# Kernel tuning notes

Hardware: AMD Instinct MI355X
Metric: run time of the kernel (lower is better)

Reference implementation:

```python
import jax, jax.numpy as jnp
import numpy as np

B, N, E = 4, 8192, 65536
OBS, H, OUT, NOUT = 128, 256, 1024, 18


def setup_inputs() -> dict:
    key = jax.random.key(0)
    ks = jax.random.split(key, 8)
    nodes = jax.random.normal(ks[0], (B, N, OBS), dtype=jnp.float32)
    edges = jax.random.randint(ks[1], (B, 2, E), 0, N, dtype=jnp.int64)
    # Glorot-ish init for weights
    W0 = jax.random.normal(ks[2], (OBS, H), dtype=jnp.float32) / np.float32(np.sqrt(OBS))
    W1 = jax.random.normal(ks[3], (H, OUT), dtype=jnp.float32) / np.float32(np.sqrt(H))
    W_logit = jax.random.normal(ks[4], (OUT, NOUT), dtype=jnp.float32) / np.float32(np.sqrt(OUT))
    W_val = jax.random.normal(ks[5], (OUT, 1), dtype=jnp.float32) / np.float32(np.sqrt(OUT))
    return {
        "nodes": nodes, "edges": edges,
        "W0": W0, "b0": jnp.zeros((H,), jnp.float32),
        "W1": W1, "b1": jnp.zeros((OUT,), jnp.float32),
        "W_logit": W_logit, "b_logit": jnp.zeros((NOUT,), jnp.float32),
        "W_val": W_val, "b_val": jnp.zeros((1,), jnp.float32),
    }


def _gcn_layer(x, src, dst, W, b, n):
    # PyG GCNConv: out = D^{-1/2} (A + I) D^{-1/2} X W + b   (self-loops already in src/dst)
    h = x @ W                                                     # [N, F_out]
    deg = jax.ops.segment_sum(jnp.ones(src.shape, jnp.float32), dst, num_segments=n)
    dinv = jnp.where(deg > 0, jax.lax.rsqrt(deg), 0.0)            # deg^{-1/2}
    norm = dinv[src] * dinv[dst]                                  # [Etot]
    msg = h[src] * norm[:, None]                                  # gather + normalize
    agg = jax.ops.segment_sum(msg, dst, num_segments=n)           # scatter-add
    return agg + b


def reference(nodes, edges, W0, b0, W1, b1, W_logit, b_logit, W_val, b_val):
    n = nodes.shape[1]
    loops = jnp.arange(n, dtype=edges.dtype)  # self-loops, added by GCNConv

    def per_graph(x, ei):
        src = jnp.concatenate([ei[0], loops])
        dst = jnp.concatenate([ei[1], loops])
        h = jax.nn.relu(_gcn_layer(x, src, dst, W0, b0, n))
        # (original applies F.dropout here; omitted for a deterministic reference)
        h = jax.nn.relu(_gcn_layer(h, src, dst, W1, b1, n))
        return h

    out = jax.vmap(per_graph)(nodes, edges)        # [B, N, OUT]
    logits = out @ W_logit + b_logit               # [B, N, NOUT]
    values = (out @ W_val + b_val)[..., 0]         # [B, N]
    return logits, values
```

## Files before the change

kernel.cpp:

```cpp
#include <hip/hip_runtime.h>
#include <hip/hip_bf16.h>

#define BB   4
#define NN   8192
#define EE   65536
#define FOBS 128
#define FH   256
#define FOUT 1024
#define NLOG 18
#define BKT  64

typedef __attribute__((ext_vector_type(8))) short frag8;
typedef __attribute__((ext_vector_type(4))) float f32x4;

__device__ __forceinline__ ushort f2b(float v) {
    __hip_bfloat16 h = __float2bfloat16(v);
    return *reinterpret_cast<ushort*>(&h);
}
__device__ __forceinline__ float blo(uint u) { return __uint_as_float(u << 16); }
__device__ __forceinline__ float bhi(uint u) { return __uint_as_float(u & 0xffff0000u); }

__device__ __forceinline__ void gld16(const void* g, void* l) {
    __builtin_amdgcn_global_load_lds(
        (const __attribute__((address_space(1))) unsigned*)g,
        (__attribute__((address_space(3))) unsigned*)l, 16, 0, 0);
}

#define XB2_N  (BB * NN * FOBS / 2)
#define W0_N   (FOBS * FH)
#define W1_N   (FH * FOUT)
#define WH_N   (19 * FOUT)
#define CUR_N  (BB * NN)
#define OUTI_N (BB * NN * 19)
#define PREP_TOTAL (XB2_N + W0_N + W1_N + WH_N + CUR_N + OUTI_N)

__global__ void prep_kernel(const float* __restrict__ nodes, uint* __restrict__ xb,
                            const float* __restrict__ W0, ushort* __restrict__ W0T,
                            const float* __restrict__ W1, ushort* __restrict__ W1T,
                            const float* __restrict__ Wl, const float* __restrict__ Wv,
                            ushort* __restrict__ WT19, int* __restrict__ cursor,
                            const float* __restrict__ bl, const float* __restrict__ bv,
                            float* __restrict__ out_logits, float* __restrict__ out_values) {
    int idx = blockIdx.x * blockDim.x + threadIdx.x;
    if (idx < XB2_N) {
        float2 xx = ((const float2*)nodes)[idx];
        xb[idx] = (uint)f2b(xx.x) | ((uint)f2b(xx.y) << 16);
        return;
    }
    idx -= XB2_N;
    if (idx < W0_N) {
        int n = idx / FOBS, k = idx - n * FOBS;
        W0T[idx] = f2b(W0[(size_t)k * FH + n]);
        return;
    }
    idx -= W0_N;
    if (idx < W1_N) {
        int n = idx / FH, k = idx - n * FH;
        W1T[idx] = f2b(W1[(size_t)k * FOUT + n]);
        return;
    }
    idx -= W1_N;
    if (idx < WH_N) {
        int o = idx >> 10, k = idx & (FOUT - 1);
        WT19[idx] = f2b((o < NLOG) ? Wl[(size_t)k * NLOG + o] : Wv[k]);
        return;
    }
    idx -= WH_N;
    if (idx < CUR_N) { cursor[idx] = 0; return; }
    idx -= CUR_N;
    if (idx < OUTI_N) {
        int gn = idx / 19, o = idx - gn * 19;
        if (o < NLOG) out_logits[(size_t)gn * NLOG + o] = bl[o];
        else          out_values[gn] = bv[0];
    }
}

__global__ void bucket_fill(const int* __restrict__ edges, int* __restrict__ cursor,
                            ushort* __restrict__ bucket) {
    int blk = blockIdx.x;
    int xcd = blk & 7;
    int g = xcd >> 1;
    int chunk = (blk >> 3) * 2 + (xcd & 1);
    int e = chunk * 256 + threadIdx.x;
    const int* src = edges + (size_t)g * 2 * EE;
    const int* dst = src + EE;
    int d = dst[e];
    int slot = atomicAdd(&cursor[(size_t)g * NN + d], 1);
    if (slot < BKT) bucket[((size_t)g * NN + d) * BKT + slot] = (ushort)src[e];
}

__global__ __launch_bounds__(256) void gather_agg_b128(
    const uint4* __restrict__ xb4_all, const int* __restrict__ cnt_all,
    const ushort* __restrict__ bucket, uint4* __restrict__ agg_all)
{
    int blk = blockIdx.x;
    int xcd = blk & 7;
    int g = xcd >> 1;
    int chunk = (blk >> 3) * 2 + (xcd & 1);
    int wv = threadIdx.x >> 6, lane = threadIdx.x & 63;
    int n = chunk * 4 + wv;
    int q = lane >> 4, sub = lane & 15;
    const uint4* xb4 = xb4_all + (size_t)g * NN * 16;
    const int* cnt = cnt_all + (size_t)g * NN;
    const ushort* bkt = bucket + ((size_t)g * NN + n) * BKT;

    int cn = cnt[n];
    float wn = rsqrtf((float)cn + 1.0f);
    int total = min(cn, BKT) + 1;

    float acc[8] = {};
    for (int base = 0; base < total; base += 8) {
#pragma unroll
        for (int j = 0; j < 2; ++j) {
            int vr = base + q + 4 * j;
            bool ok = vr < total;
            int src = (!ok || vr == 0) ? n : (int)bkt[vr - 1];
            float w = ok ? rsqrtf((float)cnt[src] + 1.0f) * wn : 0.0f;
            uint4 r = xb4[(size_t)src * 16 + sub];
            acc[0] += w * blo(r.x); acc[1] += w * bhi(r.x);
            acc[2] += w * blo(r.y); acc[3] += w * bhi(r.y);
            acc[4] += w * blo(r.z); acc[5] += w * bhi(r.z);
            acc[6] += w * blo(r.w); acc[7] += w * bhi(r.w);
        }
    }
#pragma unroll
    for (int e = 0; e < 8; ++e) {
        acc[e] += __shfl_xor(acc[e], 16);
        acc[e] += __shfl_xor(acc[e], 32);
    }
    if (lane < 16) {
        uint4 o;
        o.x = (uint)f2b(acc[0]) | ((uint)f2b(acc[1]) << 16);
        o.y = (uint)f2b(acc[2]) | ((uint)f2b(acc[3]) << 16);
        o.z = (uint)f2b(acc[4]) | ((uint)f2b(acc[5]) << 16);
        o.w = (uint)f2b(acc[6]) | ((uint)f2b(acc[7]) << 16);
        agg_all[((size_t)g * NN + n) * 16 + sub] = o;
    }
}

__global__ __launch_bounds__(256) void gather_agg_b256(
    const uint4* __restrict__ xb4_all, const int* __restrict__ cnt_all,
    const ushort* __restrict__ bucket, uint4* __restrict__ agg_all)
{
    int blk = blockIdx.x;
    int xcd = blk & 7;
    int g = xcd >> 1;
    int chunk = (blk >> 3) * 2 + (xcd & 1);
    int wv = threadIdx.x >> 6, lane = threadIdx.x & 63;
    int n = chunk * 4 + wv;
    int h = lane >> 5, sub = lane & 31;
    const uint4* xb4 = xb4_all + (size_t)g * NN * 32;
    const int* cnt = cnt_all + (size_t)g * NN;
    const ushort* bkt = bucket + ((size_t)g * NN + n) * BKT;

    int cn = cnt[n];
    float wn = rsqrtf((float)cn + 1.0f);
    int total = min(cn, BKT) + 1;

    float acc[8] = {};
    for (int base = 0; base < total; base += 8) {
#pragma unroll
        for (int j = 0; j < 4; ++j) {
            int vr = base + h + 2 * j;
            bool ok = vr < total;
            int src = (!ok || vr == 0) ? n : (int)bkt[vr - 1];
            float w = ok ? rsqrtf((float)cnt[src] + 1.0f) * wn : 0.0f;
            uint4 r = xb4[(size_t)src * 32 + sub];
            acc[0] += w * blo(r.x); acc[1] += w * bhi(r.x);
            acc[2] += w * blo(r.y); acc[3] += w * bhi(r.y);
            acc[4] += w * blo(r.z); acc[5] += w * bhi(r.z);
            acc[6] += w * blo(r.w); acc[7] += w * bhi(r.w);
        }
    }
#pragma unroll
    for (int e = 0; e < 8; ++e)
        acc[e] += __shfl_xor(acc[e], 32);
    if (lane < 32) {
        uint4 o;
        o.x = (uint)f2b(acc[0]) | ((uint)f2b(acc[1]) << 16);
        o.y = (uint)f2b(acc[2]) | ((uint)f2b(acc[3]) << 16);
        o.z = (uint)f2b(acc[4]) | ((uint)f2b(acc[5]) << 16);
        o.w = (uint)f2b(acc[6]) | ((uint)f2b(acc[7]) << 16);
        agg_all[((size_t)g * NN + n) * 32 + sub] = o;
    }
}

__global__ __launch_bounds__(256) void mfma_gemm(
    const ushort* __restrict__ A_all, const ushort* __restrict__ BT,
    const float* __restrict__ bias, ushort* __restrict__ C_all,
    int M, int N, int K, int relu)
{
    __shared__ __align__(16) ushort As[128 * 64];
    __shared__ __align__(16) ushort Bs[128 * 64];

    int g = blockIdx.z;
    const ushort* A = A_all + (size_t)g * M * K;
    ushort* C = C_all + (size_t)g * M * N;

    int t = threadIdx.x;
    int bn = blockIdx.x, bm = blockIdx.y;
    int lane = t & 63, w = t >> 6;
    int wm = w >> 1, wn = w & 1;
    int l15 = lane & 15, quad = lane >> 4;

    f32x4 acc[4][4] = {};

    const char* Abase = (const char*)(A + (size_t)(bm * 128) * K);
    const char* Bbase = (const char*)(BT + (size_t)(bn * 128) * K);
    size_t rstride = (size_t)K * 2;

    int rsub = lane >> 3;
    int colb = (lane & 7) * 16;

    for (int k0 = 0; k0 < K; k0 += 64) {
#pragma unroll
        for (int c = 0; c < 4; ++c) {
            int grp = c * 4 + w;
            int row = grp * 8 + rsub;
            int gcol = k0 * 2 + (colb ^ ((row & 7) << 4));
            gld16(Abase + (size_t)row * rstride + gcol, (char*)As + grp * 1024);
            gld16(Bbase + (size_t)row * rstride + gcol, (char*)Bs + grp * 1024);
        }
        __syncthreads();
#pragma unroll
        for (int kk = 0; kk < 64; kk += 32) {
            frag8 af[4], bf[4];
#pragma unroll
            for (int i = 0; i < 4; ++i) {
                int r = wm * 64 + i * 16 + l15;
                int cb = (kk * 2 + quad * 16) ^ ((r & 7) << 4);
                af[i] = *(const frag8*)((const char*)As + r * 128 + cb);
            }
#pragma unroll
            for (int j = 0; j < 4; ++j) {
                int r = wn * 64 + j * 16 + l15;
                int cb = (kk * 2 + quad * 16) ^ ((r & 7) << 4);
                bf[j] = *(const frag8*)((const char*)Bs + r * 128 + cb);
            }
#pragma unroll
            for (int i = 0; i < 4; ++i)
#pragma unroll
                for (int j = 0; j < 4; ++j)
                    acc[i][j] = __builtin_amdgcn_mfma_f32_16x16x32_bf16(af[i], bf[j], acc[i][j], 0, 0, 0);
        }
        __syncthreads();
    }

#pragma unroll
    for (int i = 0; i < 4; ++i) {
#pragma unroll
        for (int j = 0; j < 4; ++j) {
            int col = bn * 128 + wn * 64 + j * 16 + l15;
            float bcol = bias[col];
#pragma unroll
            for (int r = 0; r < 4; ++r) {
                int row = bm * 128 + wm * 64 + i * 16 + quad * 4 + r;
                float v = acc[i][j][r] + bcol;
                if (relu) v = fmaxf(v, 0.0f);
                C[(size_t)row * N + col] = f2b(v);
            }
        }
    }
}

__global__ __launch_bounds__(256) void gemm2_heads(
    const ushort* __restrict__ hagg_all,
    const ushort* __restrict__ W1T,
    const float*  __restrict__ b1,
    const ushort* __restrict__ WT19,
    float* __restrict__ out_logits,
    float* __restrict__ out_values)
{
    __shared__ __align__(16) ushort smem[128 * 136];
    __shared__ __align__(16) ushort wt[20][136];

    char* AsB = (char*)smem;
    char* BsB = (char*)smem + 16384;
    ushort* Ct = smem;

    int bm = blockIdx.x, sp = blockIdx.y, g = blockIdx.z;
    int t = threadIdx.x;
    int lane = t & 63, w = t >> 6;
    int wm = w >> 1, wn = w & 1;
    int l15 = lane & 15, quad = lane >> 4;

    const char* A0 = (const char*)(hagg_all + ((size_t)g * NN + bm * 128) * FH);

    if (t < 136) wt[19][t] = 0;

    int rsub = lane >> 3;
    int colb = (lane & 7) * 16;

    f32x4 hacc[2][2] = {};

    for (int bi = 0; bi < 4; ++bi) {
        int bn = sp * 4 + bi;
        __syncthreads();

        for (int idx = t; idx < 19 * 16; idx += 256) {
            int row = idx >> 4, c8 = (idx & 15) * 8;
            *(uint4*)&wt[row][c8] = *(const uint4*)(WT19 + (size_t)row * FOUT + bn * 128 + c8);
        }

        f32x4 acc[4][4] = {};
        const char* Bbase = (const char*)(W1T + (size_t)(bn * 128) * FH);

        for (int k0 = 0; k0 < FH; k0 += 64) {
#pragma unroll
            for (int c = 0; c < 4; ++c) {
                int grp = c * 4 + w;
                int row = grp * 8 + rsub;
                int gcol = k0 * 2 + (colb ^ ((row & 7) << 4));
                gld16(A0 + (size_t)row * (FH * 2) + gcol, AsB + grp * 1024);
                gld16(Bbase + (size_t)row * (FH * 2) + gcol, BsB + grp * 1024);
            }
            __syncthreads();
#pragma unroll
            for (int kk = 0; kk < 64; kk += 32) {
                frag8 af[4], bf[4];
#pragma unroll
                for (int i = 0; i < 4; ++i) {
                    int r = wm * 64 + i * 16 + l15;
                    int cb = (kk * 2 + quad * 16) ^ ((r & 7) << 4);
                    af[i] = *(const frag8*)(AsB + r * 128 + cb);
                }
#pragma unroll
                for (int j = 0; j < 4; ++j) {
                    int r = wn * 64 + j * 16 + l15;
                    int cb = (kk * 2 + quad * 16) ^ ((r & 7) << 4);
                    bf[j] = *(const frag8*)(BsB + r * 128 + cb);
                }
#pragma unroll
                for (int i = 0; i < 4; ++i)
#pragma unroll
                    for (int j = 0; j < 4; ++j)
                        acc[i][j] = __builtin_amdgcn_mfma_f32_16x16x32_bf16(af[i], bf[j], acc[i][j], 0, 0, 0);
            }
            __syncthreads();
        }

#pragma unroll
        for (int j = 0; j < 4; ++j) {
            int colL = wn * 64 + j * 16 + l15;
            float bcol = b1[bn * 128 + colL];
#pragma unroll
            for (int i = 0; i < 4; ++i) {
                int rowL = wm * 64 + i * 16 + quad * 4;
#pragma unroll
                for (int r = 0; r < 4; ++r) {
                    float v = fmaxf(acc[i][j][r] + bcol, 0.0f);
                    Ct[(size_t)(rowL + r) * 136 + colL] = f2b(v);
                }
            }
        }
        __syncthreads();

        int r1 = (l15 < 3) ? (16 + l15) : 19;
#pragma unroll
        for (int kk = 0; kk < 128; kk += 32) {
            frag8 b0 = *(const frag8*)&wt[l15][kk + quad * 8];
            frag8 bO = *(const frag8*)&wt[r1][kk + quad * 8];
#pragma unroll
            for (int mt = 0; mt < 2; ++mt) {
                int row = (w * 2 + mt) * 16 + l15;
                frag8 af = *(const frag8*)&Ct[(size_t)row * 136 + kk + quad * 8];
                hacc[mt][0] = __builtin_amdgcn_mfma_f32_16x16x32_bf16(af, b0, hacc[mt][0], 0, 0, 0);
                hacc[mt][1] = __builtin_amdgcn_mfma_f32_16x16x32_bf16(af, bO, hacc[mt][1], 0, 0, 0);
            }
        }
    }

#pragma unroll
    for (int mt = 0; mt < 2; ++mt) {
#pragma unroll
        for (int r = 0; r < 4; ++r) {
            int node = bm * 128 + (w * 2 + mt) * 16 + quad * 4 + r;
            size_t gn = (size_t)g * NN + node;
            atomicAdd(&out_logits[gn * NLOG + l15], hacc[mt][0][r]);
            if (l15 < 2)       atomicAdd(&out_logits[gn * NLOG + 16 + l15], hacc[mt][1][r]);
            else if (l15 == 2) atomicAdd(&out_values[gn], hacc[mt][1][r]);
        }
    }
}

extern "C" void kernel_launch(void* const* d_in, const int* in_sizes, int n_in,
                              void* d_out, int out_size, void* d_ws, size_t ws_size,
                              hipStream_t stream) {
    const float* nodes = (const float*)d_in[0];
    const int*   edges = (const int*)d_in[1];
    const float* W0 = (const float*)d_in[2];
    const float* b0 = (const float*)d_in[3];
    const float* W1 = (const float*)d_in[4];
    const float* b1 = (const float*)d_in[5];
    const float* Wl = (const float*)d_in[6];
    const float* bl = (const float*)d_in[7];
    const float* Wv = (const float*)d_in[8];
    const float* bv = (const float*)d_in[9];

    float* out_logits = (float*)d_out;
    float* out_values = out_logits + (size_t)BB * NN * NLOG;

    char* ws = (char*)d_ws;
    int*    cursor  = (int*)(ws);
    ushort* W0T     = (ushort*)(ws + (128 << 10));
    ushort* W1T     = (ushort*)(ws + (192 << 10));
    ushort* WT19    = (ushort*)(ws + (704 << 10));
    uint*   xb      = (uint*)(ws + (1u << 20));
    ushort* bucket  = (ushort*)(ws + (9u << 20));
    ushort* xagg_b  = (ushort*)(ws + (13u << 20));
    ushort* h1b     = (ushort*)(ws + (21u << 20));
    ushort* hagg_b  = (ushort*)(ws + (37u << 20));

    prep_kernel<<<(PREP_TOTAL + 255) / 256, 256, 0, stream>>>(
        nodes, xb, W0, W0T, W1, W1T, Wl, Wv, WT19, cursor, bl, bv, out_logits, out_values);

    bucket_fill<<<1024, 256, 0, stream>>>(edges, cursor, bucket);

    gather_agg_b128<<<(NN / 4) * BB, 256, 0, stream>>>((const uint4*)xb, cursor, bucket,
                                                       (uint4*)xagg_b);

    mfma_gemm<<<dim3(FH / 128, NN / 128, BB), 256, 0, stream>>>(
        xagg_b, W0T, b0, h1b, NN, FH, FOBS, 1);

    gather_agg_b256<<<(NN / 4) * BB, 256, 0, stream>>>((const uint4*)h1b, cursor, bucket,
                                                       (uint4*)hagg_b);

    gemm2_heads<<<dim3(NN / 128, 2, BB), 256, 0, stream>>>(hagg_b, W1T, b1, WT19,
                                                           out_logits, out_values);
}
```

Measured before the change: 181.3 us.

## Double-buffer LDS tiles in both MFMA GEMM kernels to overlap loads with compute

The generic GEMM gets two LDS buffers so the next K-tile is loaded asynchronously while the current one feeds the MFMAs, which removes one barrier per K step. The fused GEMM+heads kernel is flattened into a 16-step loop over column blocks and K-tiles. It ping-pongs between a new 32 KB buffer and the existing Ct buffer, so prefetch of the next tile overlaps compute, including across column-block boundaries. The cost is more LDS per block (about 64 KB and over 70 KB), which may lower occupancy. It also makes the reuse of the Ct region as a prefetch buffer depend on careful ordering of stages and barriers.

After: 186.0 us. +2.6%, slower.

```diff
diff --git a/kernel.cpp b/kernel.cpp
--- a/kernel.cpp
+++ b/kernel.cpp
@@ -190,8 +190,8 @@
     const float* __restrict__ bias, ushort* __restrict__ C_all,
     int M, int N, int K, int relu)
 {
-    __shared__ __align__(16) ushort As[128 * 64];
-    __shared__ __align__(16) ushort Bs[128 * 64];
+    __shared__ __align__(16) char As[2][16384];
+    __shared__ __align__(16) char Bs[2][16384];
 
     int g = blockIdx.z;
     const ushort* A = A_all + (size_t)g * M * K;
@@ -212,16 +212,26 @@
     int rsub = lane >> 3;
     int colb = (lane & 7) * 16;
 
-    for (int k0 = 0; k0 < K; k0 += 64) {
-#pragma unroll
-        for (int c = 0; c < 4; ++c) {
-            int grp = c * 4 + w;
-            int row = grp * 8 + rsub;
-            int gcol = k0 * 2 + (colb ^ ((row & 7) << 4));
-            gld16(Abase + (size_t)row * rstride + gcol, (char*)As + grp * 1024);
-            gld16(Bbase + (size_t)row * rstride + gcol, (char*)Bs + grp * 1024);
-        }
-        __syncthreads();
+#define G1_STAGE(buf, k0v)                                                        \
+    {                                                                             \
+        _Pragma("unroll")                                                         \
+        for (int c = 0; c < 4; ++c) {                                             \
+            int grp = c * 4 + w;                                                  \
+            int row = grp * 8 + rsub;                                             \
+            int gcol = (k0v) * 2 + (colb ^ ((row & 7) << 4));                     \
+            gld16(Abase + (size_t)row * rstride + gcol, As[buf] + grp * 1024);    \
+            gld16(Bbase + (size_t)row * rstride + gcol, Bs[buf] + grp * 1024);    \
+        }                                                                         \
+    }
+
+    G1_STAGE(0, 0);
+    __syncthreads();
+
+    int nsteps = K >> 6;
+    for (int s = 0; s < nsteps; ++s) {
+        if (s + 1 < nsteps) G1_STAGE((s + 1) & 1, (s + 1) * 64);
+        const char* Ab = As[s & 1];
+        const char* Bb = Bs[s & 1];
 #pragma unroll
         for (int kk = 0; kk < 64; kk += 32) {
             frag8 af[4], bf[4];
@@ -229,13 +239,13 @@
             for (int i = 0; i < 4; ++i) {
                 int r = wm * 64 + i * 16 + l15;
                 int cb = (kk * 2 + quad * 16) ^ ((r & 7) << 4);
-                af[i] = *(const frag8*)((const char*)As + r * 128 + cb);
+                af[i] = *(const frag8*)(Ab + r * 128 + cb);
             }
 #pragma unroll
             for (int j = 0; j < 4; ++j) {
                 int r = wn * 64 + j * 16 + l15;
                 int cb = (kk * 2 + quad * 16) ^ ((r & 7) << 4);
-                bf[j] = *(const frag8*)((const char*)Bs + r * 128 + cb);
+                bf[j] = *(const frag8*)(Bb + r * 128 + cb);
             }
 #pragma unroll
             for (int i = 0; i < 4; ++i)
@@ -272,10 +282,9 @@
     float* __restrict__ out_values)
 {
     __shared__ __align__(16) ushort smem[128 * 136];
+    __shared__ __align__(16) char pbuf0[32768];
     __shared__ __align__(16) ushort wt[20][136];
 
-    char* AsB = (char*)smem;
-    char* BsB = (char*)smem + 16384;
     ushort* Ct = smem;
 
     int bm = blockIdx.x, sp = blockIdx.y, g = blockIdx.z;
@@ -283,90 +292,110 @@
     int lane = t & 63, w = t >> 6;
     int wm = w >> 1, wn = w & 1;
     int l15 = lane & 15, quad = lane >> 4;
-
-    const char* A0 = (const char*)(hagg_all + ((size_t)g * NN + bm * 128) * FH);
-
-    if (t < 136) wt[19][t] = 0;
-
     int rsub = lane >> 3;
     int colb = (lane & 7) * 16;
 
+    const char* A0 = (const char*)(hagg_all + ((size_t)g * NN + bm * 128) * FH);
+
+#define G2_STAGE(dst, sv)                                                          \
+    {                                                                              \
+        char* Pb_ = (dst);                                                         \
+        int bn_ = sp * 4 + ((sv) >> 2);                                            \
+        int k0_ = ((sv) & 3) * 64;                                                 \
+        const char* Bb_ = (const char*)(W1T + (size_t)(bn_ * 128) * FH);           \
+        _Pragma("unroll")                                                          \
+        for (int c = 0; c < 4; ++c) {                                              \
+            int grp = c * 4 + w;                                                   \
+            int row = grp * 8 + rsub;                                              \
+            int gcol = k0_ * 2 + (colb ^ ((row & 7) << 4));                        \
+            gld16(A0 + (size_t)row * (FH * 2) + gcol, Pb_ + grp * 1024);           \
+            gld16(Bb_ + (size_t)row * (FH * 2) + gcol, Pb_ + 16384 + grp * 1024);  \
+        }                                                                          \
+    }
+
+    if (t < 136) wt[19][t] = 0;
+    G2_STAGE(pbuf0, 0);
+    __syncthreads();
+
     f32x4 hacc[2][2] = {};
-
-    for (int bi = 0; bi < 4; ++bi) {
+    f32x4 acc[4][4] = {};
+
+    for (int s = 0; s < 16; ++s) {
+        int bi = s >> 2, k0i = s & 3;
         int bn = sp * 4 + bi;
+
+        if (k0i == 0) {
+            for (int idx = t; idx < 19 * 16; idx += 256) {
+                int row = idx >> 4, c8 = (idx & 15) * 8;
+                *(uint4*)&wt[row][c8] = *(const uint4*)(WT19 + (size_t)row * FOUT + bn * 128 + c8);
+            }
+        }
+        if (s < 15) {
+            char* nb = ((s + 1) & 1) ? (char*)smem : pbuf0;
+            G2_STAGE(nb, s + 1);
+        }
+
+        const char* Ab = (s & 1) ? (const char*)smem : (const char*)pbuf0;
+        const char* Bb = Ab + 16384;
+#pragma unroll
+        for (int kk = 0; kk < 64; kk += 32) {
+            frag8 af[4], bf[4];
+#pragma unroll
+            for (int i = 0; i < 4; ++i) {
+                int r = wm * 64 + i * 16 + l15;
+                int cb = (kk * 2 + quad * 16) ^ ((r & 7) << 4);
+                af[i] = *(const frag8*)(Ab + r * 128 + cb);
+            }
+#pragma unroll
+            for (int j = 0; j < 4; ++j) {
+                int r = wn * 64 + j * 16 + l15;
+                int cb = (kk * 2 + quad * 16) ^ ((r & 7) << 4);
+                bf[j] = *(const frag8*)(Bb + r * 128 + cb);
+            }
+#pragma unroll
+            for (int i = 0; i < 4; ++i)
+#pragma unroll
+                for (int j = 0; j < 4; ++j)
+                    acc[i][j] = __builtin_amdgcn_mfma_f32_16x16x32_bf16(af[i], bf[j], acc[i][j], 0, 0, 0);
+        }
         __syncthreads();
 
-        for (int idx = t; idx < 19 * 16; idx += 256) {
-            int row = idx >> 4, c8 = (idx & 15) * 8;
-            *(uint4*)&wt[row][c8] = *(const uint4*)(WT19 + (size_t)row * FOUT + bn * 128 + c8);
-        }
-
-        f32x4 acc[4][4] = {};
-        const char* Bbase = (const char*)(W1T + (size_t)(bn * 128) * FH);
-
-        for (int k0 = 0; k0 < FH; k0 += 64) {
-#pragma unroll
-            for (int c = 0; c < 4; ++c) {
-                int grp = c * 4 + w;
-                int row = grp * 8 + rsub;
-                int gcol = k0 * 2 + (colb ^ ((row & 7) << 4));
-                gld16(A0 + (size_t)row * (FH * 2) + gcol, AsB + grp * 1024);
-                gld16(Bbase + (size_t)row * (FH * 2) + gcol, BsB + grp * 1024);
-            }
+        if (k0i == 3) {
+#pragma unroll
+            for (int j = 0; j < 4; ++j) {
+                int colL = wn * 64 + j * 16 + l15;
+                float bcol = b1[bn * 128 + colL];
+#pragma unroll
+                for (int i = 0; i < 4; ++i) {
+                    int rowL = wm * 64 + i * 16 + quad * 4;
+#pragma unroll
+                    for (int r = 0; r < 4; ++r) {
+                        float v = fmaxf(acc[i][j][r] + bcol, 0.0f);
+                        Ct[(size_t)(rowL + r) * 136 + colL] = f2b(v);
+                    }
+                }
+            }
+#pragma unroll
+            for (int i = 0; i < 4; ++i)
+#pragma unroll
+                for (int j = 0; j < 4; ++j)
+                    acc[i][j] = f32x4{0.f, 0.f, 0.f, 0.f};
             __syncthreads();
-#pragma unroll
-            for (int kk = 0; kk < 64; kk += 32) {
-                frag8 af[4], bf[4];
-#pragma unroll
-                for (int i = 0; i < 4; ++i) {
-                    int r = wm * 64 + i * 16 + l15;
-                    int cb = (kk * 2 + quad * 16) ^ ((r & 7) << 4);
-                    af[i] = *(const frag8*)(AsB + r * 128 + cb);
+
+            int r1 = (l15 < 3) ? (16 + l15) : 19;
+#pragma unroll
+            for (int kk = 0; kk < 128; kk += 32) {
+                frag8 b0 = *(const frag8*)&wt[l15][kk + quad * 8];
+                frag8 bO = *(const frag8*)&wt[r1][kk + quad * 8];
+#pragma unroll
+                for (int mt = 0; mt < 2; ++mt) {
+                    int row = (w * 2 + mt) * 16 + l15;
+                    frag8 af = *(const frag8*)&Ct[(size_t)row * 136 + kk + quad * 8];
+                    hacc[mt][0] = __builtin_amdgcn_mfma_f32_16x16x32_bf16(af, b0, hacc[mt][0], 0, 0, 0);
+                    hacc[mt][1] = __builtin_amdgcn_mfma_f32_16x16x32_bf16(af, bO, hacc[mt][1], 0, 0, 0);
                 }
-#pragma unroll
-                for (int j = 0; j < 4; ++j) {
-                    int r = wn * 64 + j * 16 + l15;
-                    int cb = (kk * 2 + quad * 16) ^ ((r & 7) << 4);
-                    bf[j] = *(const frag8*)(BsB + r * 128 + cb);
-                }
-#pragma unroll
-                for (int i = 0; i < 4; ++i)
-#pragma unroll
-                    for (int j = 0; j < 4; ++j)
-                        acc[i][j] = __builtin_amdgcn_mfma_f32_16x16x32_bf16(af[i], bf[j], acc[i][j], 0, 0, 0);
             }
             __syncthreads();
-        }
-
-#pragma unroll
-        for (int j = 0; j < 4; ++j) {
-            int colL = wn * 64 + j * 16 + l15;
-            float bcol = b1[bn * 128 + colL];
-#pragma unroll
-            for (int i = 0; i < 4; ++i) {
-                int rowL = wm * 64 + i * 16 + quad * 4;
-#pragma unroll
-                for (int r = 0; r < 4; ++r) {
-                    float v = fmaxf(acc[i][j][r] + bcol, 0.0f);
-                    Ct[(size_t)(rowL + r) * 136 + colL] = f2b(v);
-                }
-            }
-        }
-        __syncthreads();
-
-        int r1 = (l15 < 3) ? (16 + l15) : 19;
-#pragma unroll
-        for (int kk = 0; kk < 128; kk += 32) {
-            frag8 b0 = *(const frag8*)&wt[l15][kk + quad * 8];
-            frag8 bO = *(const frag8*)&wt[r1][kk + quad * 8];
-#pragma unroll
-            for (int mt = 0; mt < 2; ++mt) {
-                int row = (w * 2 + mt) * 16 + l15;
-                frag8 af = *(const frag8*)&Ct[(size_t)row * 136 + kk + quad * 8];
-                hacc[mt][0] = __builtin_amdgcn_mfma_f32_16x16x32_bf16(af, b0, hacc[mt][0], 0, 0, 0);
-                hacc[mt][1] = __builtin_amdgcn_mfma_f32_16x16x32_bf16(af, bO, hacc[mt][1], 0, 0, 0);
-            }
         }
     }
 
```
